# Performance work log

Measured on AMD Instinct MI355X. Metric: run time of the kernel, lower is better.

The kernel has to match this reference:

```python
import jax, jax.numpy as jnp
import numpy as np
import math

N, T, D, H = 8, 1024, 768, 12

def setup_inputs() -> dict:
    key = jax.random.key(0)
    ks = jax.random.split(key, 5)
    s = 1.0 / math.sqrt(D)
    return {
        "x": jax.random.normal(ks[0], (N, T, D), dtype=jnp.float32),
        "Wq": jax.random.normal(ks[1], (D, D), dtype=jnp.float32) * s,
        "Wk": jax.random.normal(ks[2], (D, D), dtype=jnp.float32) * s,
        "Wv": jax.random.normal(ks[3], (D, D), dtype=jnp.float32) * s,
        "Wo": jax.random.normal(ks[4], (D, D), dtype=jnp.float32) * s,
        "bo": jnp.zeros((D,), dtype=jnp.float32),
    }

def reference(x, Wq, Wk, Wv, Wo, bo):
    n, t, d = x.shape
    h = H
    dh = d // h  # 64
    # nn.Linear: y = x @ W.T
    q = (x @ Wq.T).reshape(n, t, h, dh).transpose(0, 2, 1, 3)  # [n,h,t,dh]
    k = (x @ Wk.T).reshape(n, t, h, dh).transpose(0, 2, 1, 3)
    v = (x @ Wv.T).reshape(n, t, h, dh).transpose(0, 2, 1, 3)
    scores = jnp.einsum('nhqd,nhkd->nhqk', q, k) / math.sqrt(dh)  # [n,h,t,t]
    causal = jnp.tril(jnp.ones((t, t), dtype=bool))
    scores = jnp.where(causal, scores, -jnp.inf)
    attn = jax.nn.softmax(scores, axis=-1)
    out = jnp.einsum('nhqk,nhkd->nhqd', attn, v)  # [n,h,t,dh]
    out = out.transpose(0, 2, 1, 3).reshape(n, t, d)
    return out @ Wo.T + bo
```

## Files before the change

kernel.cpp:

```cpp
#include <hip/hip_runtime.h>

typedef __attribute__((ext_vector_type(8))) short short8;
typedef __attribute__((ext_vector_type(4))) float f32x4;
typedef __attribute__((ext_vector_type(4))) short short4v;
typedef __attribute__((ext_vector_type(4))) unsigned short ushort4v;

#define DEV static __device__ __forceinline__

DEV unsigned short f2bf(float f) {
  unsigned int u = __builtin_bit_cast(unsigned int, f);
  u += 0x7fffu + ((u >> 16) & 1u);
  return (unsigned short)(u >> 16);
}

DEV unsigned int pack2bf(float a, float b) {
  return (unsigned int)f2bf(a) | ((unsigned int)f2bf(b) << 16);
}

DEV void gload16(const void* g, void* l) {
  __builtin_amdgcn_global_load_lds(
      (const __attribute__((address_space(1))) unsigned int*)g,
      (__attribute__((address_space(3))) unsigned int*)l, 16, 0, 0);
}

__global__ __launch_bounds__(256) void cvt_bf16(const float* __restrict__ in,
                                                unsigned short* __restrict__ out,
                                                int nvec4) {
  int i = blockIdx.x * 256 + threadIdx.x;
  if (i >= nvec4) return;
  float4 v = ((const float4*)in)[i];
  ushort4v o = {f2bf(v.x), f2bf(v.y), f2bf(v.z), f2bf(v.w)};
  *(ushort4v*)(out + (size_t)i * 4) = o;
}

__global__ __launch_bounds__(256) void cvt_w4(const float* __restrict__ w0,
                                              const float* __restrict__ w1,
                                              const float* __restrict__ w2,
                                              const float* __restrict__ w3,
                                              unsigned short* __restrict__ out) {
  int i = blockIdx.x * 256 + threadIdx.x;
  int wsel = i / 147456;
  int j = i - wsel * 147456;
  const float* src = wsel == 0 ? w0 : wsel == 1 ? w1 : wsel == 2 ? w2 : w3;
  float4 v = ((const float4*)src)[j];
  ushort4v o = {f2bf(v.x), f2bf(v.y), f2bf(v.z), f2bf(v.w)};
  *(ushort4v*)(out + (size_t)i * 4) = o;
}

__global__ __launch_bounds__(256) void gemm_qkv(const short* __restrict__ A,
                                                const short* __restrict__ B0,
                                                unsigned short* __restrict__ QK,
                                                unsigned short* __restrict__ Vt) {
  __shared__ short As[2][128 * 32];
  __shared__ short Bs[2][128 * 32];
  const int tid = threadIdx.x;
  const int lane = tid & 63;
  const int wave = tid >> 6;
  const int row0 = blockIdx.x * 128;
  const int wsel = blockIdx.y / 6;
  const int col0 = (blockIdx.y % 6) * 128;
  const short* B = B0 + (size_t)wsel * 589824;
  const int wr = (wave >> 1) * 64;
  const int wc = (wave & 1) * 64;

  f32x4 acc[4][4] = {};

  const short* aG = A + (size_t)(row0 + wave * 16 + (lane >> 2)) * 768 + (lane & 3) * 8;
  const short* bG = B + (size_t)(col0 + wave * 16 + (lane >> 2)) * 768 + (lane & 3) * 8;
  char* aL = (char*)&As[0][0] + wave * 1024;
  char* bL = (char*)&Bs[0][0] + wave * 1024;

  const int cl = lane & 15;
  const int g8 = (lane >> 4) * 8;

#define QKV_STAGE(buf, kk)                          \
  do {                                              \
    gload16(aG + (kk), aL + (buf)*8192);            \
    gload16(aG + 64 * 768 + (kk), aL + (buf)*8192 + 4096); \
    gload16(bG + (kk), bL + (buf)*8192);            \
    gload16(bG + 64 * 768 + (kk), bL + (buf)*8192 + 4096); \
  } while (0)

#define QKV_COMPUTE(buf)                                                          \
  do {                                                                            \
    short8 af[4], bfr[4];                                                         \
    _Pragma("unroll") for (int m = 0; m < 4; m++)                                 \
        af[m] = *(const short8*)&As[buf][(wr + m * 16 + cl) * 32 + g8];           \
    _Pragma("unroll") for (int n = 0; n < 4; n++)                                 \
        bfr[n] = *(const short8*)&Bs[buf][(wc + n * 16 + cl) * 32 + g8];          \
    _Pragma("unroll") for (int m = 0; m < 4; m++)                                 \
        _Pragma("unroll") for (int n = 0; n < 4; n++)                             \
            acc[m][n] = __builtin_amdgcn_mfma_f32_16x16x32_bf16(af[m], bfr[n],    \
                                                                acc[m][n], 0, 0, 0); \
  } while (0)

  QKV_STAGE(0, 0);
  __syncthreads();
  int cur = 0;
  for (int kk = 32; kk < 768; kk += 32) {
    QKV_STAGE(cur ^ 1, kk);
    QKV_COMPUTE(cur);
    __syncthreads();
    cur ^= 1;
  }
  QKV_COMPUTE(cur);

  const int r4 = (lane >> 4) * 4;
  unsigned short* Qout = QK + (size_t)wsel * 6291456;
#pragma unroll
  for (int m = 0; m < 4; m++) {
#pragma unroll
    for (int n = 0; n < 4; n++) {
      const int row = row0 + wr + m * 16 + r4;
      const int col = col0 + wc + n * 16 + cl;
      if (wsel < 2) {
#pragma unroll
        for (int r = 0; r < 4; r++) {
          Qout[(size_t)(((((row + r) >> 10) * 12 + (col >> 6)) << 16) +
                        (((row + r) & 1023) << 6) + (col & 63))] = f2bf(acc[m][n][r]);
        }
      } else {
        short4v ov;
#pragma unroll
        for (int r = 0; r < 4; r++) ov[r] = (short)f2bf(acc[m][n][r]);
        *(short4v*)((short*)Vt + (size_t)((((row >> 10) * 12 + (col >> 6)) << 16) +
                                          ((col & 63) << 10) + (row & 1023))) = ov;
      }
    }
  }
}

__global__ __launch_bounds__(256) void gemm_out(const short* __restrict__ A,
                                                const short* __restrict__ B,
                                                float* __restrict__ Cout,
                                                const float* __restrict__ bias) {
  __shared__ short As[2][128 * 32];
  __shared__ short Bs[2][128 * 32];
  const int tid = threadIdx.x;
  const int lane = tid & 63;
  const int wave = tid >> 6;
  const int row0 = blockIdx.x * 128;
  const int col0 = blockIdx.y * 128;
  const int wr = (wave >> 1) * 64;
  const int wc = (wave & 1) * 64;

  f32x4 acc[4][4] = {};

  const short* aG = A + (size_t)(row0 + wave * 16 + (lane >> 2)) * 768 + (lane & 3) * 8;
  const short* bG = B + (size_t)(col0 + wave * 16 + (lane >> 2)) * 768 + (lane & 3) * 8;
  char* aL = (char*)&As[0][0] + wave * 1024;
  char* bL = (char*)&Bs[0][0] + wave * 1024;

  const int cl = lane & 15;
  const int g8 = (lane >> 4) * 8;

  QKV_STAGE(0, 0);
  __syncthreads();
  int cur = 0;
  for (int kk = 32; kk < 768; kk += 32) {
    QKV_STAGE(cur ^ 1, kk);
    QKV_COMPUTE(cur);
    __syncthreads();
    cur ^= 1;
  }
  QKV_COMPUTE(cur);

  const int r4 = (lane >> 4) * 4;
#pragma unroll
  for (int m = 0; m < 4; m++) {
#pragma unroll
    for (int n = 0; n < 4; n++) {
#pragma unroll
      for (int r = 0; r < 4; r++) {
        const int row = row0 + wr + m * 16 + r4 + r;
        const int col = col0 + wc + n * 16 + cl;
        Cout[(size_t)row * 768 + col] = acc[m][n][r] + bias[col];
      }
    }
  }
}

__global__ __launch_bounds__(256) void attn_fwd(const short* __restrict__ Qh,
                                                const short* __restrict__ Kh,
                                                const short* __restrict__ Vt,
                                                short* __restrict__ Obuf) {
  __shared__ short Ks[32 * 72];
  __shared__ short Vs[64 * 40];
  __shared__ unsigned int Ps[4][16 * 36];

  const int tid = threadIdx.x;
  const int lane = tid & 63;
  const int w = tid >> 6;
  const int nh = blockIdx.y;
  const int nIdx = nh / 12;
  const int hIdx = nh % 12;
  const int hb = nh << 16;
  const int qloc = lane & 15;
  const int g = lane >> 4;
  const int kRow = tid >> 3, kColB = (tid & 7) * 8;
  const int vRow = tid >> 2, vColB = (tid & 3) * 8;

  for (int rep = 0; rep < 2; rep++) {
    const int qb = rep ? (15 - blockIdx.x) : blockIdx.x;
    const int qr0 = qb * 64 + w * 16;
    const int qg = qr0 + qloc;
    const int qmax = qr0 + 15;
    const int kv_end = qb * 64 + 64;

    short8 qf[2];
    qf[0] = *(const short8*)&Qh[hb + qg * 64 + g * 8];
    qf[1] = *(const short8*)&Qh[hb + qg * 64 + 32 + g * 8];

    float m_run = -INFINITY, l_run = 0.f;
    f32x4 o[4] = {};

    for (int kv0 = 0; kv0 < kv_end; kv0 += 32) {
      *(short8*)&Ks[kRow * 72 + kColB] = *(const short8*)&Kh[hb + (kv0 + kRow) * 64 + kColB];
      *(short8*)&Vs[vRow * 40 + vColB] = *(const short8*)&Vt[hb + vRow * 1024 + kv0 + vColB];
      __syncthreads();
      if (kv0 <= qmax) {
        f32x4 s[2] = {};
#pragma unroll
        for (int c = 0; c < 2; c++) {
          short8 a0 = *(const short8*)&Ks[qloc * 72 + c * 32 + g * 8];
          short8 a1 = *(const short8*)&Ks[(16 + qloc) * 72 + c * 32 + g * 8];
          s[0] = __builtin_amdgcn_mfma_f32_16x16x32_bf16(a0, qf[c], s[0], 0, 0, 0);
          s[1] = __builtin_amdgcn_mfma_f32_16x16x32_bf16(a1, qf[c], s[1], 0, 0, 0);
        }
        float pv[2][4];
        float pm = -INFINITY;
#pragma unroll
        for (int kt = 0; kt < 2; kt++)
#pragma unroll
          for (int r = 0; r < 4; r++) {
            const int kg = kv0 + kt * 16 + g * 4 + r;
            float sv = s[kt][r] * 0.125f;
            sv = (kg <= qg) ? sv : -INFINITY;
            pv[kt][r] = sv;
            pm = fmaxf(pm, sv);
          }
        pm = fmaxf(pm, __shfl_xor(pm, 16));
        pm = fmaxf(pm, __shfl_xor(pm, 32));
        const float mnew = fmaxf(m_run, pm);
        const float corr = __expf(m_run - mnew);
        float lsum = 0.f;
#pragma unroll
        for (int kt = 0; kt < 2; kt++)
#pragma unroll
          for (int r = 0; r < 4; r++) {
            float p = __expf(pv[kt][r] - mnew);
            pv[kt][r] = p;
            lsum += p;
          }
        lsum += __shfl_xor(lsum, 16);
        lsum += __shfl_xor(lsum, 32);
        l_run = l_run * corr + lsum;
        m_run = mnew;
#pragma unroll
        for (int dt = 0; dt < 4; dt++) o[dt] *= corr;
        unsigned int* pr = &Ps[w][qloc * 36];
#pragma unroll
        for (int kt = 0; kt < 2; kt++) {
          pr[kt * 8 + g * 2] = pack2bf(pv[kt][0], pv[kt][1]);
          pr[kt * 8 + g * 2 + 1] = pack2bf(pv[kt][2], pv[kt][3]);
        }
        __asm__ volatile("" ::: "memory");
        short8 pf = *(const short8*)((const short*)&Ps[w][0] + qloc * 72 + g * 8);
#pragma unroll
        for (int dt = 0; dt < 4; dt++) {
          short8 vf = *(const short8*)&Vs[(dt * 16 + qloc) * 40 + g * 8];
          o[dt] = __builtin_amdgcn_mfma_f32_16x16x32_bf16(vf, pf, o[dt], 0, 0, 0);
        }
      }
      __syncthreads();
    }

    const float inv = 1.f / l_run;
    const int outRow = nIdx * 1024 + qr0 + qloc;
    short* op = Obuf + (size_t)outRow * 768 + hIdx * 64;
#pragma unroll
    for (int dt = 0; dt < 4; dt++) {
      short4v ov;
#pragma unroll
      for (int r = 0; r < 4; r++) ov[r] = (short)f2bf(o[dt][r] * inv);
      *(short4v*)(op + dt * 16 + g * 4) = ov;
    }
  }
}

extern "C" void kernel_launch(void* const* d_in, const int* in_sizes, int n_in,
                              void* d_out, int out_size, void* d_ws, size_t ws_size,
                              hipStream_t stream) {
  (void)in_sizes; (void)n_in; (void)out_size; (void)ws_size;
  const float* x  = (const float*)d_in[0];
  const float* Wq = (const float*)d_in[1];
  const float* Wk = (const float*)d_in[2];
  const float* Wv = (const float*)d_in[3];
  const float* Wo = (const float*)d_in[4];
  const float* bo = (const float*)d_in[5];

  char* ws = (char*)d_ws;
  short* xb  = (short*)(ws);
  short* wqb = (short*)(ws + 12582912);
  short* wob = (short*)(ws + 12582912 + 3 * 1179648);
  short* Qh  = (short*)(ws + 17301504);
  short* Kh  = (short*)(ws + 17301504 + 12582912);
  short* Vt  = (short*)(ws + 17301504 + 2 * 12582912);
  short* Ob  = (short*)(ws + 17301504 + 3 * 12582912);

  cvt_bf16<<<6144, 256, 0, stream>>>(x, (unsigned short*)xb, 1572864);
  cvt_w4<<<2304, 256, 0, stream>>>(Wq, Wk, Wv, Wo, (unsigned short*)wqb);

  gemm_qkv<<<dim3(64, 18), 256, 0, stream>>>(xb, wqb, (unsigned short*)Qh,
                                             (unsigned short*)Vt);

  attn_fwd<<<dim3(8, 96), 256, 0, stream>>>(Qh, Kh, Vt, Ob);

  gemm_out<<<dim3(64, 6), 256, 0, stream>>>(Ob, wob, (float*)d_out, bo);
}
```

Baseline: 204.8 us.

## Split attention KV range across two wave groups and merge partial softmax states

Doubles the attention block to 512 threads, with two groups of four waves each processing half of the KV tiles for the same query block. The groups then merge their partial (m, l, O) states through shared memory. The change also switches to exp2 with the scale folded in, skips causal masking on fully-visible tiles, and skips the rescale when the running max does not grow much (lazy rescaling). This aims to raise parallelism and cut exp and mask work, at the cost of an extra merge step with syncs and more shared memory per block.

```diff
diff --git a/kernel.cpp b/kernel.cpp
--- a/kernel.cpp
+++ b/kernel.cpp
@@ -180,32 +180,41 @@
   }
 }
 
-__global__ __launch_bounds__(256) void attn_fwd(const short* __restrict__ Qh,
+__global__ __launch_bounds__(512) void attn_fwd(const short* __restrict__ Qh,
                                                 const short* __restrict__ Kh,
                                                 const short* __restrict__ Vt,
                                                 short* __restrict__ Obuf) {
-  __shared__ short Ks[32 * 72];
-  __shared__ short Vs[64 * 40];
-  __shared__ unsigned int Ps[4][16 * 36];
+  __shared__ short Ks[2][32 * 72];
+  __shared__ short Vs[2][64 * 40];
+  __shared__ unsigned int Ps[8][16 * 36];
 
   const int tid = threadIdx.x;
   const int lane = tid & 63;
-  const int w = tid >> 6;
+  const int wave = tid >> 6;
+  const int w4 = wave & 3;
+  const int gg = wave >> 2;
+  const int t8 = tid & 255;
   const int nh = blockIdx.y;
   const int nIdx = nh / 12;
   const int hIdx = nh % 12;
   const int hb = nh << 16;
   const int qloc = lane & 15;
   const int g = lane >> 4;
-  const int kRow = tid >> 3, kColB = (tid & 7) * 8;
-  const int vRow = tid >> 2, vColB = (tid & 3) * 8;
-
-  for (int rep = 0; rep < 2; rep++) {
-    const int qb = rep ? (15 - blockIdx.x) : blockIdx.x;
-    const int qr0 = qb * 64 + w * 16;
+  const int kRow = t8 >> 3, kColB = (t8 & 7) * 8;
+  const int vRow = t8 >> 2, vColB = (t8 & 3) * 8;
+  short* KsG = &Ks[gg][0];
+  short* VsG = &Vs[gg][0];
+  float* Mbuf = (float*)&Ps[0][0];
+  float* slot = Mbuf + (size_t)(w4 * 64 + lane) * 18;
+
+  const float SCL = 0.18033688f;
+
+  for (int p = 0; p < 2; p++) {
+    const int qb = p ? (15 - (int)blockIdx.x) : (int)blockIdx.x;
+    const int nsteps = qb + 1;
+    const int qr0 = qb * 64 + w4 * 16;
     const int qg = qr0 + qloc;
     const int qmax = qr0 + 15;
-    const int kv_end = qb * 64 + 64;
 
     short8 qf[2];
     qf[0] = *(const short8*)&Qh[hb + qg * 64 + g * 8];
@@ -214,77 +223,121 @@
     float m_run = -INFINITY, l_run = 0.f;
     f32x4 o[4] = {};
 
-    for (int kv0 = 0; kv0 < kv_end; kv0 += 32) {
-      *(short8*)&Ks[kRow * 72 + kColB] = *(const short8*)&Kh[hb + (kv0 + kRow) * 64 + kColB];
-      *(short8*)&Vs[vRow * 40 + vColB] = *(const short8*)&Vt[hb + vRow * 1024 + kv0 + vColB];
+    for (int s = 0; s < nsteps; s++) {
+      const int kv0 = (s + gg * nsteps) * 32;
+      *(short8*)&KsG[kRow * 72 + kColB] = *(const short8*)&Kh[hb + (kv0 + kRow) * 64 + kColB];
+      *(short8*)&VsG[vRow * 40 + vColB] = *(const short8*)&Vt[hb + vRow * 1024 + kv0 + vColB];
       __syncthreads();
       if (kv0 <= qmax) {
-        f32x4 s[2] = {};
+        f32x4 s2[2] = {};
 #pragma unroll
         for (int c = 0; c < 2; c++) {
-          short8 a0 = *(const short8*)&Ks[qloc * 72 + c * 32 + g * 8];
-          short8 a1 = *(const short8*)&Ks[(16 + qloc) * 72 + c * 32 + g * 8];
-          s[0] = __builtin_amdgcn_mfma_f32_16x16x32_bf16(a0, qf[c], s[0], 0, 0, 0);
-          s[1] = __builtin_amdgcn_mfma_f32_16x16x32_bf16(a1, qf[c], s[1], 0, 0, 0);
+          short8 a0 = *(const short8*)&KsG[qloc * 72 + c * 32 + g * 8];
+          short8 a1 = *(const short8*)&KsG[(16 + qloc) * 72 + c * 32 + g * 8];
+          s2[0] = __builtin_amdgcn_mfma_f32_16x16x32_bf16(a0, qf[c], s2[0], 0, 0, 0);
+          s2[1] = __builtin_amdgcn_mfma_f32_16x16x32_bf16(a1, qf[c], s2[1], 0, 0, 0);
         }
         float pv[2][4];
         float pm = -INFINITY;
-#pragma unroll
-        for (int kt = 0; kt < 2; kt++)
-#pragma unroll
-          for (int r = 0; r < 4; r++) {
-            const int kg = kv0 + kt * 16 + g * 4 + r;
-            float sv = s[kt][r] * 0.125f;
-            sv = (kg <= qg) ? sv : -INFINITY;
-            pv[kt][r] = sv;
-            pm = fmaxf(pm, sv);
-          }
+        if (kv0 + 31 <= qr0) {
+#pragma unroll
+          for (int kt = 0; kt < 2; kt++)
+#pragma unroll
+            for (int r = 0; r < 4; r++) {
+              float sv = s2[kt][r] * SCL;
+              pv[kt][r] = sv;
+              pm = fmaxf(pm, sv);
+            }
+        } else {
+#pragma unroll
+          for (int kt = 0; kt < 2; kt++)
+#pragma unroll
+            for (int r = 0; r < 4; r++) {
+              const int kg = kv0 + kt * 16 + g * 4 + r;
+              float sv = s2[kt][r] * SCL;
+              sv = (kg <= qg) ? sv : -INFINITY;
+              pv[kt][r] = sv;
+              pm = fmaxf(pm, sv);
+            }
+        }
         pm = fmaxf(pm, __shfl_xor(pm, 16));
         pm = fmaxf(pm, __shfl_xor(pm, 32));
-        const float mnew = fmaxf(m_run, pm);
-        const float corr = __expf(m_run - mnew);
-        float lsum = 0.f;
-#pragma unroll
-        for (int kt = 0; kt < 2; kt++)
-#pragma unroll
-          for (int r = 0; r < 4; r++) {
-            float p = __expf(pv[kt][r] - mnew);
-            pv[kt][r] = p;
-            lsum += p;
-          }
-        lsum += __shfl_xor(lsum, 16);
-        lsum += __shfl_xor(lsum, 32);
-        l_run = l_run * corr + lsum;
-        m_run = mnew;
-#pragma unroll
-        for (int dt = 0; dt < 4; dt++) o[dt] *= corr;
-        unsigned int* pr = &Ps[w][qloc * 36];
+        if (__all(pm <= m_run + 11.5f)) {
+          float lsum = 0.f;
+#pragma unroll
+          for (int kt = 0; kt < 2; kt++)
+#pragma unroll
+            for (int r = 0; r < 4; r++) {
+              float pp = exp2f(pv[kt][r] - m_run);
+              pv[kt][r] = pp;
+              lsum += pp;
+            }
+          lsum += __shfl_xor(lsum, 16);
+          lsum += __shfl_xor(lsum, 32);
+          l_run += lsum;
+        } else {
+          const float mnew = fmaxf(m_run, pm);
+          const float corr = exp2f(m_run - mnew);
+          float lsum = 0.f;
+#pragma unroll
+          for (int kt = 0; kt < 2; kt++)
+#pragma unroll
+            for (int r = 0; r < 4; r++) {
+              float pp = exp2f(pv[kt][r] - mnew);
+              pv[kt][r] = pp;
+              lsum += pp;
+            }
+          lsum += __shfl_xor(lsum, 16);
+          lsum += __shfl_xor(lsum, 32);
+          l_run = l_run * corr + lsum;
+          m_run = mnew;
+#pragma unroll
+          for (int dt = 0; dt < 4; dt++) o[dt] *= corr;
+        }
+        unsigned int* pr = &Ps[wave][qloc * 36];
 #pragma unroll
         for (int kt = 0; kt < 2; kt++) {
           pr[kt * 8 + g * 2] = pack2bf(pv[kt][0], pv[kt][1]);
           pr[kt * 8 + g * 2 + 1] = pack2bf(pv[kt][2], pv[kt][3]);
         }
         __asm__ volatile("" ::: "memory");
-        short8 pf = *(const short8*)((const short*)&Ps[w][0] + qloc * 72 + g * 8);
+        short8 pf = *(const short8*)((const short*)&Ps[wave][0] + qloc * 72 + g * 8);
 #pragma unroll
         for (int dt = 0; dt < 4; dt++) {
-          short8 vf = *(const short8*)&Vs[(dt * 16 + qloc) * 40 + g * 8];
+          short8 vf = *(const short8*)&VsG[(dt * 16 + qloc) * 40 + g * 8];
           o[dt] = __builtin_amdgcn_mfma_f32_16x16x32_bf16(vf, pf, o[dt], 0, 0, 0);
         }
       }
       __syncthreads();
     }
 
-    const float inv = 1.f / l_run;
-    const int outRow = nIdx * 1024 + qr0 + qloc;
-    short* op = Obuf + (size_t)outRow * 768 + hIdx * 64;
-#pragma unroll
-    for (int dt = 0; dt < 4; dt++) {
-      short4v ov;
-#pragma unroll
-      for (int r = 0; r < 4; r++) ov[r] = (short)f2bf(o[dt][r] * inv);
-      *(short4v*)(op + dt * 16 + g * 4) = ov;
-    }
+    if (gg == 1) {
+#pragma unroll
+      for (int dt = 0; dt < 4; dt++)
+#pragma unroll
+        for (int r = 0; r < 4; r++) slot[dt * 4 + r] = o[dt][r];
+      slot[16] = m_run;
+      slot[17] = l_run;
+    }
+    __syncthreads();
+    if (gg == 0) {
+      const float m1 = slot[16], l1 = slot[17];
+      const float mm = fmaxf(m_run, m1);
+      const float c0 = exp2f(m_run - mm);
+      const float c1 = exp2f(m1 - mm);
+      const float inv = 1.f / (l_run * c0 + l1 * c1);
+      const int outRow = nIdx * 1024 + qr0 + qloc;
+      short* op = Obuf + (size_t)outRow * 768 + hIdx * 64;
+#pragma unroll
+      for (int dt = 0; dt < 4; dt++) {
+        short4v ov;
+#pragma unroll
+        for (int r = 0; r < 4; r++)
+          ov[r] = (short)f2bf((o[dt][r] * c0 + slot[dt * 4 + r] * c1) * inv);
+        *(short4v*)(op + dt * 16 + g * 4) = ov;
+      }
+    }
+    __syncthreads();
   }
 }
 
@@ -314,7 +367,7 @@
   gemm_qkv<<<dim3(64, 18), 256, 0, stream>>>(xb, wqb, (unsigned short*)Qh,
                                              (unsigned short*)Vt);
 
-  attn_fwd<<<dim3(8, 96), 256, 0, stream>>>(Qh, Kh, Vt, Ob);
+  attn_fwd<<<dim3(8, 96), 512, 0, stream>>>(Qh, Kh, Vt, Ob);
 
   gemm_out<<<dim3(64, 6), 256, 0, stream>>>(Ob, wob, (float*)d_out, bo);
 }
```

After: 210.1 us. +2.6%, slower.
